# Kernel optimization log

Hardware: AMD Instinct MI355X
Metric: run time of the kernel (lower is better)

The kernel has to match this reference:

```python
import math
import jax, jax.numpy as jnp
import numpy as np

EPS = 1e-8

def setup_inputs() -> dict:
    key = jax.random.key(0)
    k1, k2, k3, k4 = jax.random.split(key, 4)
    B, Cin, Cout, K, S, H, W = 8, 512, 512, 3, 512, 64, 64
    return {
        "x": jax.random.normal(k1, (B, Cin, H, W), dtype=jnp.float32),
        "style": jax.random.normal(k2, (B, S), dtype=jnp.float32),
        "weight": jax.random.normal(k3, (1, Cout, Cin, K, K), dtype=jnp.float32),
        "mod_weight": jax.random.normal(k4, (Cin, S), dtype=jnp.float32),
        "mod_bias": jnp.ones((Cin,), dtype=jnp.float32),
    }


def reference(x, style, weight, mod_weight, mod_bias):
    B, Cin, H, W = x.shape
    _, Cout, _, K, _ = weight.shape
    S = mod_weight.shape[1]
    lin_scale = 1.0 / math.sqrt(S)          # EqualLinear scale (lr_mul=1)
    conv_scale = 1.0 / math.sqrt(Cin * K * K)  # fan_in scale
    pad = K // 2

    # modulation: EqualLinear(style) -> [B, Cin], reshaped to [B,1,Cin,1,1]
    s = style @ (mod_weight * lin_scale).T + mod_bias
    s5 = s[:, None, :, None, None]

    # per-sample modulated weight [B, Cout, Cin, K, K]
    w = conv_scale * weight * s5
    demod = jax.lax.rsqrt(jnp.sum(w * w, axis=(2, 3, 4)) + EPS)  # [B, Cout]
    w = w * demod[:, :, None, None, None]

    # batch-as-groups conv: x -> [1, B*Cin, H, W], w -> [B*Cout, Cin, K, K]
    xg = x.reshape(1, B * Cin, H, W)
    wg = w.reshape(B * Cout, Cin, K, K)
    out = jax.lax.conv_general_dilated(
        xg, wg,
        window_strides=(1, 1),
        padding=[(pad, pad), (pad, pad)],
        dimension_numbers=("NCHW", "OIHW", "NCHW"),
        feature_group_count=B,
    )
    out = out.reshape(B, Cout, H, W)
    return out, s5
```

## Files before the change

### kernel.cpp

```cpp
#include <hip/hip_runtime.h>
#include <hip/hip_bf16.h>


typedef __attribute__((ext_vector_type(8))) short short8;
typedef __attribute__((ext_vector_type(4))) float f32x4;

#define LIN_SCALE 0.04419417382415922f
#define CONV_SCALE 0.014731391274719739f
#define CONV_SCALE2 (1.0f/4608.0f)
#define OUT_IMG (8*512*64*64)

static __device__ __forceinline__ unsigned short f2bf(float f) {
    union { float f; unsigned int u; } a; a.f = f;
    unsigned int u = a.u;
    return (unsigned short)((u + 0x7fffu + ((u >> 16) & 1u)) >> 16);
}
static __device__ __forceinline__ short8 as_s8(uint4 v) {
    union { uint4 u; short8 s; } x; x.u = v; return x.s;
}

__global__ __launch_bounds__(256) void k_style(const float* __restrict__ style,
                                               const float* __restrict__ mw,
                                               const float* __restrict__ mb,
                                               float* __restrict__ s_ws,
                                               float* __restrict__ out_s5) {
    int wid = blockIdx.x * 4 + (threadIdx.x >> 6);
    int lane = threadIdx.x & 63;
    int b = wid >> 9, ci = wid & 511;
    float sum = 0.f;
    for (int k = lane; k < 512; k += 64)
        sum += style[b*512 + k] * mw[ci*512 + k];
    for (int off = 32; off > 0; off >>= 1) sum += __shfl_xor(sum, off);
    if (lane == 0) {
        float v = sum * LIN_SCALE + mb[ci];
        s_ws[b*512 + ci] = v;
        out_s5[b*512 + ci] = v;
    }
}

__global__ __launch_bounds__(256) void k_wprep(const float* __restrict__ weight,
                                               unsigned short* __restrict__ wfrag) {
    __shared__ float wsh[4608];
    int co = blockIdx.x;
    int cog = co >> 4, l15 = co & 15;
    for (int i = threadIdx.x; i < 4608; i += 256) wsh[i] = weight[co*4608 + i];
    __syncthreads();
    uint4* wf4 = (uint4*)wfrag;
    for (int idx = threadIdx.x; idx < 576; idx += 256) {
        int t = idx / 64;
        int rem = idx & 63;
        int cig = rem >> 2, lg = rem & 3;
        union { unsigned short h[8]; uint4 v; } u;
        #pragma unroll
        for (int j = 0; j < 8; ++j)
            u.h[j] = f2bf(wsh[(cig*32 + lg*8 + j)*9 + t] * CONV_SCALE);
        wf4[((t*16 + cig)*32 + cog)*64 + lg*16 + l15] = u.v;
    }
}

__global__ __launch_bounds__(256) void k_demod(const float* __restrict__ weight,
                                               const float* __restrict__ s_ws,
                                               float* __restrict__ demod) {
    __shared__ float s2[4096];
    __shared__ float red[4][8];
    int co = blockIdx.x;
    for (int i = threadIdx.x; i < 4096; i += 256) { float v = s_ws[i]; s2[i] = v*v; }
    __syncthreads();
    float acc[8] = {0,0,0,0,0,0,0,0};
    for (int idx = threadIdx.x; idx < 4608; idx += 256) {
        float w = weight[co*4608 + idx];
        float w2 = w*w;
        int ci = idx / 9;
        #pragma unroll
        for (int b = 0; b < 8; ++b) acc[b] += w2 * s2[b*512 + ci];
    }
    int lane = threadIdx.x & 63, wv = threadIdx.x >> 6;
    #pragma unroll
    for (int b = 0; b < 8; ++b) {
        float v = acc[b];
        for (int off = 32; off > 0; off >>= 1) v += __shfl_xor(v, off);
        if (lane == 0) red[wv][b] = v;
    }
    __syncthreads();
    if (threadIdx.x < 8) {
        float t = red[0][threadIdx.x] + red[1][threadIdx.x]
                + red[2][threadIdx.x] + red[3][threadIdx.x];
        demod[threadIdx.x*512 + co] = rsqrtf(t * CONV_SCALE2 + 1e-8f);
    }
}

__global__ __launch_bounds__(256) void k_xprep(const float* __restrict__ x,
                                               const float* __restrict__ s_ws,
                                               unsigned short* __restrict__ xs) {
    __shared__ unsigned short tile[32 * 520];
    int w0 = blockIdx.x * 32, h = blockIdx.y, b = blockIdx.z;
    int t = threadIdx.x;
    int wl = t & 31, cih = t >> 5;
    for (int ci0 = 0; ci0 < 512; ci0 += 8) {
        int ci = ci0 + cih;
        float sv = s_ws[b*512 + ci];
        float v = x[((b*512 + ci)*64 + h)*64 + (w0 + wl)] * sv;
        tile[wl*520 + ci] = f2bf(v);
    }
    __syncthreads();
    int lane = t & 63, wv = t >> 6;
    const uint4* t4 = (const uint4*)tile;
    uint4* xs4 = (uint4*)xs;
    for (int w = wv; w < 32; w += 4) {
        uint4 v = t4[w*65 + lane];
        xs4[((b*64 + h)*64 + (w0 + w))*64 + lane] = v;
    }
}

__global__ __launch_bounds__(256, 2) void k_conv(const unsigned short* __restrict__ xs,
                                                 const unsigned short* __restrict__ wfrag,
                                                 const float* __restrict__ demod,
                                                 float* __restrict__ out) {
    __shared__ uint4 lds[1056];
    int cot = blockIdx.x;
    int r0  = blockIdx.y * 2;
    int b   = blockIdx.z;
    int tid = threadIdx.x;
    int lane = tid & 63, wid = tid >> 6;
    int l15 = lane & 15, lg = lane >> 4;
    int cobase = cot*256 + wid*64;
    int cog0 = cobase >> 4;

    const uint4* xs4 = (const uint4*)xs;
    const uint4* wf4 = (const uint4*)wfrag;

    f32x4 acc[4][8];
    #pragma unroll
    for (int i = 0; i < 4; ++i)
        #pragma unroll
        for (int j = 0; j < 8; ++j) acc[i][j] = (f32x4){0.f,0.f,0.f,0.f};

    int sg  = tid & 3;
    int sc  = 1 + (tid >> 2);
    int scm1 = tid >> 2;
    const uint4* xrow = xs4 + ((b*64 + (r0 - 1))*64 + scm1)*64 + sg;

    uint4 st[4];
    auto issue = [&](int cq) {
        #pragma unroll
        for (int k = 0; k < 4; ++k) {
            int rin = r0 - 1 + k;
            st[k] = (uint4){0u,0u,0u,0u};
            if ((unsigned)rin < 64u) st[k] = xrow[k*4096 + cq];
        }
    };

    if (tid < 32) {
        int q = tid & 15;
        int col = (tid >> 4) ? 65 : 0;
        lds[q*66 + col] = (uint4){0u,0u,0u,0u};
    }
    issue(0);

    #pragma unroll 1
    for (int step = 0; step < 16; ++step) {
        __syncthreads();
        #pragma unroll
        for (int k = 0; k < 4; ++k)
            lds[(k*4 + sg)*66 + sc] = st[k];
        __syncthreads();
        if (step < 15) issue((step+1) * 4);

        #pragma unroll
        for (int kh = 0; kh < 3; ++kh) {
            #pragma unroll
            for (int kw = 0; kw < 3; ++kw) {
                int t = kh*3 + kw;
                short8 a[4], bx[8];
                #pragma unroll
                for (int nf = 0; nf < 8; ++nf) {
                    int rt = (nf >> 2) + kh;
                    int slot = (rt*4 + lg)*66 + (nf & 3)*16 + kw + l15;
                    bx[nf] = as_s8(lds[slot]);
                }
                #pragma unroll
                for (int mf = 0; mf < 4; ++mf)
                    a[mf] = as_s8(wf4[((t*16 + step)*32 + cog0 + mf)*64 + lane]);
                #pragma unroll
                for (int mf = 0; mf < 4; ++mf)
                    #pragma unroll
                    for (int nf = 0; nf < 8; ++nf)
                        acc[mf][nf] = __builtin_amdgcn_mfma_f32_16x16x32_bf16(
                            a[mf], bx[nf], acc[mf][nf], 0, 0, 0);
            }
        }
    }

    const float* dmp = demod + b*512;
    #pragma unroll
    for (int mf = 0; mf < 4; ++mf) {
        #pragma unroll
        for (int reg = 0; reg < 4; ++reg) {
            int co = cobase + mf*16 + lg*4 + reg;
            float dm = dmp[co];
            #pragma unroll
            for (int nf = 0; nf < 8; ++nf) {
                int r = r0 + (nf >> 2);
                int c = (nf & 3)*16 + l15;
                out[((b*512 + co)*64 + r)*64 + c] = acc[mf][nf][reg] * dm;
            }
        }
    }
}

extern "C" void kernel_launch(void* const* d_in, const int* in_sizes, int n_in,
                              void* d_out, int out_size, void* d_ws, size_t ws_size,
                              hipStream_t stream) {
    const float* x      = (const float*)d_in[0];
    const float* style  = (const float*)d_in[1];
    const float* weight = (const float*)d_in[2];
    const float* mw     = (const float*)d_in[3];
    const float* mb     = (const float*)d_in[4];
    float* out = (float*)d_out;

    float* s_ws           = (float*)d_ws;
    float* demod_ws       = (float*)((char*)d_ws + 16384);
    unsigned short* wfrag = (unsigned short*)((char*)d_ws + 32768);
    unsigned short* xs    = (unsigned short*)((char*)d_ws + 4751360);

    k_style<<<1024, 256, 0, stream>>>(style, mw, mb, s_ws, out + OUT_IMG);
    k_wprep<<<512, 256, 0, stream>>>(weight, wfrag);
    k_demod<<<512, 256, 0, stream>>>(weight, s_ws, demod_ws);
    k_xprep<<<dim3(2, 64, 8), 256, 0, stream>>>(x, s_ws, xs);
    k_conv<<<dim3(2, 32, 8), 256, 0, stream>>>(xs, wfrag, demod_ws, out);
}
```

Before: 272.1 us.

## Double-buffer conv LDS tiles, prefetch weight fragments, fuse wprep with demod

The conv kernel now uses two LDS buffers for the input tile, so each step needs one barrier instead of two. The next tile is written to the spare buffer mid-step, and global loads run two steps ahead. Weight A-fragments are register double-buffered and prefetched one tap ahead to hide global load latency behind MFMAs. Separately, the weight-prep and demod kernels are fused so the weights are read once and one launch is saved. The cost is more LDS and register pressure, which may reduce occupancy at 2 blocks/SM.

```diff
diff --git a/kernel.cpp b/kernel.cpp
--- a/kernel.cpp
+++ b/kernel.cpp
@@ -38,12 +38,17 @@
     }
 }
 
-__global__ __launch_bounds__(256) void k_wprep(const float* __restrict__ weight,
-                                               unsigned short* __restrict__ wfrag) {
+__global__ __launch_bounds__(256) void k_wd(const float* __restrict__ weight,
+                                            const float* __restrict__ s_ws,
+                                            unsigned short* __restrict__ wfrag,
+                                            float* __restrict__ demod) {
     __shared__ float wsh[4608];
+    __shared__ float s2[4096];
+    __shared__ float red[4][8];
     int co = blockIdx.x;
-    int cog = co >> 4, l15 = co & 15;
+    int cog = co >> 4, l15c = co & 15;
     for (int i = threadIdx.x; i < 4608; i += 256) wsh[i] = weight[co*4608 + i];
+    for (int i = threadIdx.x; i < 4096; i += 256) { float v = s_ws[i]; s2[i] = v*v; }
     __syncthreads();
     uint4* wf4 = (uint4*)wfrag;
     for (int idx = threadIdx.x; idx < 576; idx += 256) {
@@ -54,21 +59,11 @@
         #pragma unroll
         for (int j = 0; j < 8; ++j)
             u.h[j] = f2bf(wsh[(cig*32 + lg*8 + j)*9 + t] * CONV_SCALE);
-        wf4[((t*16 + cig)*32 + cog)*64 + lg*16 + l15] = u.v;
-    }
-}
-
-__global__ __launch_bounds__(256) void k_demod(const float* __restrict__ weight,
-                                               const float* __restrict__ s_ws,
-                                               float* __restrict__ demod) {
-    __shared__ float s2[4096];
-    __shared__ float red[4][8];
-    int co = blockIdx.x;
-    for (int i = threadIdx.x; i < 4096; i += 256) { float v = s_ws[i]; s2[i] = v*v; }
-    __syncthreads();
+        wf4[((t*16 + cig)*32 + cog)*64 + lg*16 + l15c] = u.v;
+    }
     float acc[8] = {0,0,0,0,0,0,0,0};
     for (int idx = threadIdx.x; idx < 4608; idx += 256) {
-        float w = weight[co*4608 + idx];
+        float w = wsh[idx];
         float w2 = w*w;
         int ci = idx / 9;
         #pragma unroll
@@ -116,7 +111,7 @@
                                                  const unsigned short* __restrict__ wfrag,
                                                  const float* __restrict__ demod,
                                                  float* __restrict__ out) {
-    __shared__ uint4 lds[1056];
+    __shared__ uint4 lds[2][1056];
     int cot = blockIdx.x;
     int r0  = blockIdx.y * 2;
     int b   = blockIdx.z;
@@ -150,45 +145,56 @@
         }
     };
 
-    if (tid < 32) {
+    short8 a[2][4];
+    auto loadA = [&](int s, int t, short8* dst) {
+        #pragma unroll
+        for (int mf = 0; mf < 4; ++mf)
+            dst[mf] = as_s8(wf4[((t*16 + s)*32 + cog0 + mf)*64 + lane]);
+    };
+
+    if (tid < 64) {
         int q = tid & 15;
-        int col = (tid >> 4) ? 65 : 0;
-        lds[q*66 + col] = (uint4){0u,0u,0u,0u};
-    }
+        int col = ((tid >> 4) & 1) ? 65 : 0;
+        lds[tid >> 5][q*66 + col] = (uint4){0u,0u,0u,0u};
+    }
+
     issue(0);
+    #pragma unroll
+    for (int k = 0; k < 4; ++k)
+        lds[0][(k*4 + sg)*66 + sc] = st[k];
+    issue(4);
+    loadA(0, 0, a[0]);
+    __syncthreads();
 
     #pragma unroll 1
     for (int step = 0; step < 16; ++step) {
+        int p = step & 1;
+        #pragma unroll
+        for (int t = 0; t < 9; ++t) {
+            const int kh = t / 3, kw = t % 3;
+            if (t < 8) loadA(step, t + 1, a[(t + 1) & 1]);
+            short8 bx[8];
+            #pragma unroll
+            for (int nf = 0; nf < 8; ++nf) {
+                int rt = (nf >> 2) + kh;
+                int slot = (rt*4 + lg)*66 + (nf & 3)*16 + kw + l15;
+                bx[nf] = as_s8(lds[p][slot]);
+            }
+            if (t == 4 && step < 15) {
+                #pragma unroll
+                for (int k = 0; k < 4; ++k)
+                    lds[p ^ 1][(k*4 + sg)*66 + sc] = st[k];
+                if (step < 14) issue((step + 2) * 4);
+            }
+            #pragma unroll
+            for (int mf = 0; mf < 4; ++mf)
+                #pragma unroll
+                for (int nf = 0; nf < 8; ++nf)
+                    acc[mf][nf] = __builtin_amdgcn_mfma_f32_16x16x32_bf16(
+                        a[t & 1][mf], bx[nf], acc[mf][nf], 0, 0, 0);
+        }
+        if (step < 15) loadA(step + 1, 0, a[0]);
         __syncthreads();
-        #pragma unroll
-        for (int k = 0; k < 4; ++k)
-            lds[(k*4 + sg)*66 + sc] = st[k];
-        __syncthreads();
-        if (step < 15) issue((step+1) * 4);
-
-        #pragma unroll
-        for (int kh = 0; kh < 3; ++kh) {
-            #pragma unroll
-            for (int kw = 0; kw < 3; ++kw) {
-                int t = kh*3 + kw;
-                short8 a[4], bx[8];
-                #pragma unroll
-                for (int nf = 0; nf < 8; ++nf) {
-                    int rt = (nf >> 2) + kh;
-                    int slot = (rt*4 + lg)*66 + (nf & 3)*16 + kw + l15;
-                    bx[nf] = as_s8(lds[slot]);
-                }
-                #pragma unroll
-                for (int mf = 0; mf < 4; ++mf)
-                    a[mf] = as_s8(wf4[((t*16 + step)*32 + cog0 + mf)*64 + lane]);
-                #pragma unroll
-                for (int mf = 0; mf < 4; ++mf)
-                    #pragma unroll
-                    for (int nf = 0; nf < 8; ++nf)
-                        acc[mf][nf] = __builtin_amdgcn_mfma_f32_16x16x32_bf16(
-                            a[mf], bx[nf], acc[mf][nf], 0, 0, 0);
-            }
-        }
     }
 
     const float* dmp = demod + b*512;
@@ -224,8 +230,7 @@
     unsigned short* xs    = (unsigned short*)((char*)d_ws + 4751360);
 
     k_style<<<1024, 256, 0, stream>>>(style, mw, mb, s_ws, out + OUT_IMG);
-    k_wprep<<<512, 256, 0, stream>>>(weight, wfrag);
-    k_demod<<<512, 256, 0, stream>>>(weight, s_ws, demod_ws);
+    k_wd<<<512, 256, 0, stream>>>(weight, s_ws, wfrag, demod_ws);
     k_xprep<<<dim3(2, 64, 8), 256, 0, stream>>>(x, s_ws, xs);
     k_conv<<<dim3(2, 32, 8), 256, 0, stream>>>(xs, wfrag, demod_ws, out);
 }
```

Result: slower. 304.1 us (+11.8%).
